# Kernel optimization log

Hardware: AMD Instinct MI355X
Metric: run time of the kernel (lower is better)

Reference implementation:

```python
import jax, jax.numpy as jnp
import numpy as np

B, I, C, L, KS = 16, 64, 128, 16384, 5
CA_K = 5
K_CR = 76      # crucial channels: floor(0.6*128)=76, already even
EPS = 1e-5


def conv1d(x, w, pad):
    # x: [N, Cin, L], w: [Cout, Cin, K]
    return jax.lax.conv_general_dilated(
        x, w, window_strides=(1,), padding=[(pad, pad)],
        dimension_numbers=('NCH', 'OIH', 'NCH'))


def bn(x, g, b, m, v):
    # eval-mode BatchNorm1d over channel dim of [N, C, L]
    inv = g / jnp.sqrt(v + EPS)
    return x * inv[None, :, None] + (b - m * inv)[None, :, None]


def setup_inputs() -> dict:
    key = jax.random.key(0)
    ks = jax.random.split(key, 10)
    return {
        'x': jax.random.normal(ks[0], (B, I, L), jnp.float32),
        'conv_w': jax.random.normal(ks[1], (C, I, KS), jnp.float32) / np.sqrt(I * KS).astype(np.float32),
        'conv_b': jax.random.normal(ks[2], (C,), jnp.float32) * 0.01,
        'bn_g': jnp.ones((C,), jnp.float32) + jax.random.normal(ks[3], (C,), jnp.float32) * 0.05,
        'bn_b': jax.random.normal(ks[4], (C,), jnp.float32) * 0.05,
        'bn_m': jax.random.normal(ks[5], (C,), jnp.float32) * 0.05,
        'bn_v': jnp.ones((C,), jnp.float32) + jax.random.uniform(ks[6], (C,), jnp.float32) * 0.1,
        'alpha': jnp.float32(0.5),
        'beta': jnp.float32(0.5),
        'ca_w': jax.random.normal(ks[7], (1, 1, CA_K), jnp.float32) / np.sqrt(CA_K).astype(np.float32),
        'ca_b': jnp.zeros((1,), jnp.float32),
        'sa_w': jax.random.normal(ks[8], (1, 2, 7), jnp.float32) / np.sqrt(14.0).astype(np.float32),
        'sabn_g': jnp.ones((1,), jnp.float32) + jax.random.normal(ks[9], (1,), jnp.float32) * 0.05,
        'sabn_b': jnp.zeros((1,), jnp.float32),
        'sabn_m': jnp.zeros((1,), jnp.float32),
        'sabn_v': jnp.ones((1,), jnp.float32),
    }


def reference(x, conv_w, conv_b, bn_g, bn_b, bn_m, bn_v, alpha, beta,
              ca_w, ca_b, sa_w, sabn_g, sabn_b, sabn_m, sabn_v):
    # ---- conv_layer: Conv1d + BN + ReLU ----
    f = conv1d(x, conv_w, KS // 2) + conv_b[None, :, None]      # [B,C,L]
    f = jax.nn.relu(bn(f, bn_g, bn_b, bn_m, bn_v))

    # ---- ChannelAttention ----
    F_avg = jnp.mean(f, axis=2, keepdims=True)                  # [B,C,1]
    F_max = jnp.max(f, axis=2, keepdims=True)                   # [B,C,1]
    F_add = alpha * F_avg + 0.5 * (F_avg + F_max) + beta * F_max
    z = conv1d(F_add.transpose(0, 2, 1), ca_w, CA_K // 2) + ca_b[None, :, None]  # [B,1,C]
    channel_map = jax.nn.sigmoid(z.transpose(0, 2, 1))          # [B,C,1]

    crf = f * channel_map                                       # channel refined features

    # ---- SpatialAttention: topk channel split + scatter masks ----
    cm = channel_map[:, :, 0]                                   # [B,C]
    _, idx = jax.lax.top_k(cm, K_CR)                            # [B,K_CR]
    cru = jnp.zeros_like(cm).at[jnp.arange(B)[:, None], idx].set(1.0)[:, :, None]  # [B,C,1]
    sub = 1.0 - cru

    cf = cru * crf                                              # crucial features [B,C,L]
    sf = sub * crf                                              # subcrucial features

    c_max = jnp.max(cf, axis=1, keepdims=True)                  # [B,1,L]
    c_avg = jnp.mean(cf, axis=1, keepdims=True) * (C / K_CR)
    s_max = jnp.max(sf, axis=1, keepdims=True)
    s_avg = jnp.mean(sf, axis=1, keepdims=True) * (C / (C - K_CR))

    def gate(mx, av):
        y = conv1d(jnp.concatenate([mx, av], axis=1), sa_w, 3)  # [B,1,L]
        return jax.nn.sigmoid(jax.nn.relu(bn(y, sabn_g, sabn_b, sabn_m, sabn_v)))

    A1 = gate(c_max, c_avg)
    A2 = gate(s_max, s_avg)
    return cf * A1 + sf * A2                                    # [B,C,L]
```

## Files before the change

kernel.cpp:

```cpp
#include <hip/hip_runtime.h>
#include <hip/hip_bf16.h>
#include <math.h>

#define BB 16
#define IC 64
#define CH 128
#define LL 16384
#define KS 5
#define CAK 5
#define KCR 76
#define EPSV 1e-5f
#define NLT2 256

typedef short bf16x8 __attribute__((ext_vector_type(8)));
typedef float f32x16 __attribute__((ext_vector_type(16)));

#define OFF_WPACK 0
#define OFF_BIAS2 40960
#define OFF_PSUM  (OFF_BIAS2 + CH)
#define OFF_PMAX  (OFF_PSUM + BB*CH*NLT2)
#define OFF_CM    (OFF_PMAX + BB*CH*NLT2)
#define OFF_MASK  (OFF_CM + BB*CH)
#define OFF_A1    (OFF_MASK + BB*CH)
#define OFF_A2    (OFF_A1 + BB*LL)

__device__ __forceinline__ unsigned short f2bf(float f) {
    union { float f; unsigned u; } v; v.f = f;
    return (unsigned short)((v.u + 0x7FFFu + ((v.u >> 16) & 1u)) >> 16);
}
__device__ __forceinline__ float bf2f(unsigned short h) {
    union { unsigned u; float f; } v; v.u = ((unsigned)h) << 16;
    return v.f;
}

__global__ void prep_kernel(const float* __restrict__ conv_w, const float* __restrict__ conv_b,
                            const float* __restrict__ bn_g, const float* __restrict__ bn_b,
                            const float* __restrict__ bn_m, const float* __restrict__ bn_v,
                            unsigned short* __restrict__ wpack, float* __restrict__ bias2)
{
    int e = blockIdx.x * 256 + threadIdx.x;
    if (e < 2 * 2 * 2 * 20 * 64 * 8) {
        int j    = e & 7;
        int ln   = (e >> 3) & 63;
        int rest = e >> 9;
        int s    = rest % 20;
        int mt   = (rest / 20) & 1;
        int ch2  = (rest / 40) & 1;
        int ver  = rest / 80;
        int c  = ch2 * 64 + mt * 32 + (ln & 31);
        int kk = s >> 2;
        int i  = (s & 3) * 16 + (ln >> 5) * 8 + j;
        float inv = bn_g[c] * rsqrtf(bn_v[c] + EPSV);
        float w = conv_w[(c * IC + i) * KS + kk] * inv;
        unsigned short h = f2bf(w);
        wpack[e] = (ver == 0) ? h : f2bf(w - bf2f(h));
    }
    if (e < CH) {
        float inv = bn_g[e] * rsqrtf(bn_v[e] + EPSV);
        bias2[e] = (conv_b[e] - bn_m[e]) * inv + bn_b[e];
    }
}

__global__ __launch_bounds__(256, 3)
void conv_mfma_kernel(const float* __restrict__ x,
                      const unsigned short* __restrict__ wpack,
                      const float* __restrict__ bias2,
                      float* __restrict__ f,
                      float* __restrict__ psum, float* __restrict__ pmax)
{
    __shared__ unsigned short xs[136 * 128];
    const int b   = blockIdx.x;
    const int lt  = blockIdx.y;
    const int l0  = lt * 128;
    const int tid = threadIdx.x;
    const int ln  = tid & 63;
    const int wv  = __builtin_amdgcn_readfirstlane(tid >> 6);

    const float* xb = x + (size_t)b * (IC * LL);
    const int ibase = wv * 16;
    #pragma unroll
    for (int g = 0; g < 3; ++g) {
        int row = g * 64 + ln;
        int l   = l0 - 4 + row;
        if (row < 136) {
            bool vl = (l >= 0) && (l < LL);
            float v[16];
            #pragma unroll
            for (int q = 0; q < 16; ++q)
                v[q] = vl ? xb[(size_t)(ibase + q) * LL + l] : 0.0f;
            int rs = row & 7;
            #pragma unroll
            for (int q2 = 0; q2 < 4; ++q2) {
                unsigned short h[4], lo[4];
                #pragma unroll
                for (int j = 0; j < 4; ++j) {
                    float vv = v[q2 * 4 + j];
                    h[j]  = f2bf(vv);
                    lo[j] = f2bf(vv - bf2f(h[j]));
                }
                int i0   = ibase + q2 * 4;
                int cc   = (i0 >> 3) ^ rs;
                int epos = row * 128 + cc * 8 + (i0 & 7);
                uint2 wh, wl;
                wh.x = (unsigned)h[0]  | ((unsigned)h[1]  << 16);
                wh.y = (unsigned)h[2]  | ((unsigned)h[3]  << 16);
                wl.x = (unsigned)lo[0] | ((unsigned)lo[1] << 16);
                wl.y = (unsigned)lo[2] | ((unsigned)lo[3] << 16);
                *(uint2*)&xs[epos]      = wh;
                *(uint2*)&xs[epos + 64] = wl;
            }
        }
    }
    __syncthreads();

    const int ch2  = wv >> 1;
    const int lh   = wv & 1;
    const int ln31 = ln & 31;
    const int hi   = ln >> 5;
    const int rowbase = lh * 64 + ln31 + 2;

    const unsigned short* wp  = wpack + (size_t)ln * 8;
    const unsigned short* pA0 = wp + (size_t)((ch2 * 2 + 0) * 20) * 512;
    const unsigned short* pA1 = wp + (size_t)((ch2 * 2 + 1) * 20) * 512;
    const unsigned short* pA2 = wp + (size_t)(((2 + ch2) * 2 + 0) * 20) * 512;
    const unsigned short* pA3 = wp + (size_t)(((2 + ch2) * 2 + 1) * 20) * 512;

    f32x16 acc[2][2];
    #pragma unroll
    for (int mt = 0; mt < 2; ++mt)
        #pragma unroll
        for (int nt = 0; nt < 2; ++nt)
            #pragma unroll
            for (int r = 0; r < 16; ++r) acc[mt][nt][r] = 0.0f;

    auto loadA = [&](bf16x8* Av, int s) {
        Av[0] = *(const bf16x8*)(pA0 + (size_t)s * 512);
        Av[1] = *(const bf16x8*)(pA1 + (size_t)s * 512);
        Av[2] = *(const bf16x8*)(pA2 + (size_t)s * 512);
        Av[3] = *(const bf16x8*)(pA3 + (size_t)s * 512);
    };
    auto loadB = [&](bf16x8* Bv, int s) {
        int kk = s >> 2, iq = s & 3;
        int r0 = rowbase + kk;
        int r1 = r0 + 32;
        int c0 = ((iq << 1) + hi) ^ (r0 & 7);
        int c1 = ((iq << 1) + hi) ^ (r1 & 7);
        Bv[0] = *(const bf16x8*)&xs[r0 * 128 + c0 * 8];
        Bv[1] = *(const bf16x8*)&xs[r0 * 128 + 64 + c0 * 8];
        Bv[2] = *(const bf16x8*)&xs[r1 * 128 + c1 * 8];
        Bv[3] = *(const bf16x8*)&xs[r1 * 128 + 64 + c1 * 8];
    };
    auto compute = [&](const bf16x8* Av, const bf16x8* Bv) {
        acc[0][0] = __builtin_amdgcn_mfma_f32_32x32x16_bf16(Av[0], Bv[0], acc[0][0], 0, 0, 0);
        acc[1][0] = __builtin_amdgcn_mfma_f32_32x32x16_bf16(Av[1], Bv[0], acc[1][0], 0, 0, 0);
        acc[0][0] = __builtin_amdgcn_mfma_f32_32x32x16_bf16(Av[0], Bv[1], acc[0][0], 0, 0, 0);
        acc[1][0] = __builtin_amdgcn_mfma_f32_32x32x16_bf16(Av[1], Bv[1], acc[1][0], 0, 0, 0);
        acc[0][0] = __builtin_amdgcn_mfma_f32_32x32x16_bf16(Av[2], Bv[0], acc[0][0], 0, 0, 0);
        acc[1][0] = __builtin_amdgcn_mfma_f32_32x32x16_bf16(Av[3], Bv[0], acc[1][0], 0, 0, 0);
        acc[0][1] = __builtin_amdgcn_mfma_f32_32x32x16_bf16(Av[0], Bv[2], acc[0][1], 0, 0, 0);
        acc[1][1] = __builtin_amdgcn_mfma_f32_32x32x16_bf16(Av[1], Bv[2], acc[1][1], 0, 0, 0);
        acc[0][1] = __builtin_amdgcn_mfma_f32_32x32x16_bf16(Av[0], Bv[3], acc[0][1], 0, 0, 0);
        acc[1][1] = __builtin_amdgcn_mfma_f32_32x32x16_bf16(Av[1], Bv[3], acc[1][1], 0, 0, 0);
        acc[0][1] = __builtin_amdgcn_mfma_f32_32x32x16_bf16(Av[2], Bv[2], acc[0][1], 0, 0, 0);
        acc[1][1] = __builtin_amdgcn_mfma_f32_32x32x16_bf16(Av[3], Bv[2], acc[1][1], 0, 0, 0);
    };

    bf16x8 Aa[4], Ab[4], Ba[4], Bb[4];
    loadA(Aa, 0); loadB(Ba, 0);
    for (int s2 = 0; s2 < 10; ++s2) {
        int s = 2 * s2;
        loadA(Ab, s + 1); loadB(Bb, s + 1);
        compute(Aa, Ba);
        int sn = (s + 2 < 20) ? (s + 2) : 19;
        loadA(Aa, sn); loadB(Ba, sn);
        compute(Ab, Bb);
    }

    const int lgbase = l0 + lh * 64 + ln31;
    #pragma unroll
    for (int mt = 0; mt < 2; ++mt) {
        #pragma unroll
        for (int nt = 0; nt < 2; ++nt) {
            #pragma unroll
            for (int r = 0; r < 16; ++r) {
                int c = ch2 * 64 + mt * 32 + (r & 3) + 8 * (r >> 2) + 4 * hi;
                float fv = fmaxf(acc[mt][nt][r] + bias2[c], 0.0f);
                f[((size_t)(b * CH + c)) * LL + lgbase + nt * 32] = fv;
                acc[mt][nt][r] = fv;
            }
        }
    }
    #pragma unroll
    for (int mt = 0; mt < 2; ++mt) {
        #pragma unroll
        for (int r = 0; r < 16; ++r) {
            float s = acc[mt][0][r] + acc[mt][1][r];
            float m = fmaxf(acc[mt][0][r], acc[mt][1][r]);
            #pragma unroll
            for (int off = 1; off <= 16; off <<= 1) {
                s += __shfl_xor(s, off, 64);
                m = fmaxf(m, __shfl_xor(m, off, 64));
            }
            if (ln31 == 0) {
                int c   = ch2 * 64 + mt * 32 + (r & 3) + 8 * (r >> 2) + 4 * hi;
                int lt2 = lt * 2 + lh;
                psum[(b * CH + c) * NLT2 + lt2] = s;
                pmax[(b * CH + c) * NLT2 + lt2] = m;
            }
        }
    }
}

__global__ void chan_kernel(const float* __restrict__ psum, const float* __restrict__ pmax,
                            const float* __restrict__ alpha, const float* __restrict__ beta,
                            const float* __restrict__ ca_w, const float* __restrict__ ca_b,
                            float* __restrict__ cm, float* __restrict__ maskv)
{
    int b = blockIdx.x;
    int c = threadIdx.x;
    const float* ps = psum + (b * CH + c) * NLT2;
    const float* pm = pmax + (b * CH + c) * NLT2;
    float s = 0.0f, m = 0.0f;
    for (int t = 0; t < NLT2; ++t) { s += ps[t]; m = fmaxf(m, pm[t]); }
    float favg = s * (1.0f / LL);
    float fadd = (alpha[0] + 0.5f) * favg + (beta[0] + 0.5f) * m;

    __shared__ float fa[CH];
    __shared__ float cms[CH];
    fa[c] = fadd;
    __syncthreads();

    float z = ca_b[0];
    #pragma unroll
    for (int k = 0; k < CAK; ++k) {
        int cc = c + k - 2;
        float v = (cc >= 0 && cc < CH) ? fa[cc] : 0.0f;
        z = fmaf(ca_w[k], v, z);
    }
    float cmv = 1.0f / (1.0f + expf(-z));
    cms[c] = cmv;
    __syncthreads();

    int rank = 0;
    for (int cc = 0; cc < CH; ++cc) {
        float o = cms[cc];
        rank += (o > cmv || (o == cmv && cc < c)) ? 1 : 0;
    }
    cm[b * CH + c] = cmv;
    maskv[b * CH + c] = (rank < KCR) ? 1.0f : 0.0f;
}

__global__ __launch_bounds__(256)
void stats_gate_kernel(const float* __restrict__ f, const float* __restrict__ cm,
                       const float* __restrict__ maskv, const float* __restrict__ sa_w,
                       const float* __restrict__ sabn_g, const float* __restrict__ sabn_b,
                       const float* __restrict__ sabn_m, const float* __restrict__ sabn_v,
                       float* __restrict__ A1, float* __restrict__ A2)
{
    __shared__ float cms[CH], mks[CH];
    __shared__ float st[4][264];
    int b   = blockIdx.x;
    int l0  = blockIdx.y * 256;
    int tid = threadIdx.x;
    if (tid < CH) { cms[tid] = cm[b * CH + tid]; mks[tid] = maskv[b * CH + tid]; }
    __syncthreads();

    for (int idx = tid; idx < 262; idx += 256) {
        int l = l0 - 3 + idx;
        float cmx = 0.f, csm = 0.f, smx = 0.f, ssm = 0.f;
        if (l >= 0 && l < LL) {
            const float* fb = f + (size_t)b * CH * LL + l;
            #pragma unroll 4
            for (int c = 0; c < CH; ++c) {
                float v  = fb[(size_t)c * LL] * cms[c];
                float mk = mks[c];
                float vs = v * mk;
                float vu = v - vs;
                cmx = fmaxf(cmx, vs);
                smx = fmaxf(smx, vu);
                csm += vs;
                ssm += vu;
            }
        }
        st[0][idx] = cmx;
        st[1][idx] = csm * (1.0f / KCR);
        st[2][idx] = smx;
        st[3][idx] = ssm * (1.0f / (CH - KCR));
    }
    __syncthreads();

    float inv = sabn_g[0] * rsqrtf(sabn_v[0] + EPSV);
    float bb2 = sabn_b[0] - sabn_m[0] * inv;
    float y1 = 0.f, y2 = 0.f;
    #pragma unroll
    for (int k = 0; k < 7; ++k) {
        float wm = sa_w[k], wa = sa_w[7 + k];
        y1 = fmaf(wm, st[0][tid + k], fmaf(wa, st[1][tid + k], y1));
        y2 = fmaf(wm, st[2][tid + k], fmaf(wa, st[3][tid + k], y2));
    }
    float t1 = fmaxf(y1 * inv + bb2, 0.f);
    float t2 = fmaxf(y2 * inv + bb2, 0.f);
    A1[b * LL + l0 + tid] = 1.0f / (1.0f + expf(-t1));
    A2[b * LL + l0 + tid] = 1.0f / (1.0f + expf(-t2));
}

__global__ __launch_bounds__(256)
void final_kernel(float* __restrict__ out, const float* __restrict__ cm,
                  const float* __restrict__ maskv,
                  const float* __restrict__ A1, const float* __restrict__ A2)
{
    int g = blockIdx.x * 256 + threadIdx.x;
    size_t idx4 = (size_t)g * 4;
    int l  = (int)(idx4 & (LL - 1));
    int bc = (int)(idx4 >> 14);
    int b  = bc >> 7;
    float cmv = cm[bc];
    float mk  = maskv[bc];
    const float* Ap = (mk > 0.5f) ? A1 : A2;
    float4 a = *(const float4*)&Ap[b * LL + l];
    float4 v = *(const float4*)&out[idx4];
    v.x *= cmv * a.x;
    v.y *= cmv * a.y;
    v.z *= cmv * a.z;
    v.w *= cmv * a.w;
    *(float4*)&out[idx4] = v;
}

extern "C" void kernel_launch(void* const* d_in, const int* in_sizes, int n_in,
                              void* d_out, int out_size, void* d_ws, size_t ws_size,
                              hipStream_t stream)
{
    const float* x      = (const float*)d_in[0];
    const float* conv_w = (const float*)d_in[1];
    const float* conv_b = (const float*)d_in[2];
    const float* bn_g   = (const float*)d_in[3];
    const float* bn_b   = (const float*)d_in[4];
    const float* bn_m   = (const float*)d_in[5];
    const float* bn_v   = (const float*)d_in[6];
    const float* alpha  = (const float*)d_in[7];
    const float* beta   = (const float*)d_in[8];
    const float* ca_w   = (const float*)d_in[9];
    const float* ca_b   = (const float*)d_in[10];
    const float* sa_w   = (const float*)d_in[11];
    const float* sabn_g = (const float*)d_in[12];
    const float* sabn_b = (const float*)d_in[13];
    const float* sabn_m = (const float*)d_in[14];
    const float* sabn_v = (const float*)d_in[15];

    float* out = (float*)d_out;
    float* ws  = (float*)d_ws;

    unsigned short* wpack = (unsigned short*)(ws + OFF_WPACK);
    float* bias2 = ws + OFF_BIAS2;
    float* psum  = ws + OFF_PSUM;
    float* pmax  = ws + OFF_PMAX;
    float* cmv_  = ws + OFF_CM;
    float* mskv  = ws + OFF_MASK;
    float* A1p   = ws + OFF_A1;
    float* A2p   = ws + OFF_A2;

    prep_kernel<<<320, 256, 0, stream>>>(conv_w, conv_b, bn_g, bn_b, bn_m, bn_v, wpack, bias2);

    conv_mfma_kernel<<<dim3(BB, 128), 256, 0, stream>>>(x, wpack, bias2, out, psum, pmax);

    chan_kernel<<<BB, CH, 0, stream>>>(psum, pmax, alpha, beta, ca_w, ca_b, cmv_, mskv);

    stats_gate_kernel<<<dim3(BB, 64), 256, 0, stream>>>(out, cmv_, mskv, sa_w,
                                                        sabn_g, sabn_b, sabn_m, sabn_v, A1p, A2p);

    final_kernel<<<(BB * CH * LL / 4 + 255) / 256, 256, 0, stream>>>(out, cmv_, mskv, A1p, A2p);
}
```

Before: 190.7 us.

## Fuse spatial gate with final scaling and persist conv blocks over four tiles

The conv kernel now handles four consecutive 128-wide L tiles per block. It double-buffers the shared x staging so the next tile's global loads overlap the epilogue, keeps the channel sums and maxes in registers, and writes 3-element halo values to a side buffer. The stats/gate kernel and the final scaling kernel are merged into one kernel. It caches each 256-column slab of f in shared memory as fp16, reads halo columns from the side buffer, and writes the output in place. This removes a full extra read and write pass over f plus the A1/A2 buffers. In exchange it adds fp16 rounding of the intermediate features and raises the shared memory each block needs.

```diff
diff --git a/kernel.cpp b/kernel.cpp
--- a/kernel.cpp
+++ b/kernel.cpp
@@ -10,7 +10,7 @@
 #define CAK 5
 #define KCR 76
 #define EPSV 1e-5f
-#define NLT2 256
+#define NLT2 64
 
 typedef short bf16x8 __attribute__((ext_vector_type(8)));
 typedef float f32x16 __attribute__((ext_vector_type(16)));
@@ -21,8 +21,7 @@
 #define OFF_PMAX  (OFF_PSUM + BB*CH*NLT2)
 #define OFF_CM    (OFF_PMAX + BB*CH*NLT2)
 #define OFF_MASK  (OFF_CM + BB*CH)
-#define OFF_A1    (OFF_MASK + BB*CH)
-#define OFF_A2    (OFF_A1 + BB*LL)
+#define OFF_HB    (OFF_MASK + BB*CH)
 
 __device__ __forceinline__ unsigned short f2bf(float f) {
     union { float f; unsigned u; } v; v.f = f;
@@ -31,6 +30,14 @@
 __device__ __forceinline__ float bf2f(unsigned short h) {
     union { unsigned u; float f; } v; v.u = ((unsigned)h) << 16;
     return v.f;
+}
+__device__ __forceinline__ unsigned short f2h(float f) {
+    _Float16 h = (_Float16)f;
+    return __builtin_bit_cast(unsigned short, h);
+}
+__device__ __forceinline__ float h2f(unsigned short u) {
+    _Float16 h = __builtin_bit_cast(_Float16, u);
+    return (float)h;
 }
 
 __global__ void prep_kernel(const float* __restrict__ conv_w, const float* __restrict__ conv_b,
@@ -61,33 +68,35 @@
     }
 }
 
-__global__ __launch_bounds__(256, 3)
+__global__ __launch_bounds__(256, 2)
 void conv_mfma_kernel(const float* __restrict__ x,
                       const unsigned short* __restrict__ wpack,
                       const float* __restrict__ bias2,
                       float* __restrict__ f,
-                      float* __restrict__ psum, float* __restrict__ pmax)
+                      float* __restrict__ psum, float* __restrict__ pmax,
+                      float* __restrict__ hb)
 {
-    __shared__ unsigned short xs[136 * 128];
-    const int b   = blockIdx.x;
-    const int lt  = blockIdx.y;
-    const int l0  = lt * 128;
+    __shared__ unsigned short xs[2 * 136 * 128];
+    const int ltg = blockIdx.x;
+    const int b   = blockIdx.y;
     const int tid = threadIdx.x;
     const int ln  = tid & 63;
     const int wv  = __builtin_amdgcn_readfirstlane(tid >> 6);
+    const int ibase = wv * 16;
 
     const float* xb = x + (size_t)b * (IC * LL);
-    const int ibase = wv * 16;
-    #pragma unroll
-    for (int g = 0; g < 3; ++g) {
+
+    auto sld = [&](float* v, int l0t, int g) {
         int row = g * 64 + ln;
-        int l   = l0 - 4 + row;
+        int l   = l0t - 4 + row;
+        bool vl = (row < 136) && (l >= 0) && (l < LL);
+        #pragma unroll
+        for (int q = 0; q < 16; ++q)
+            v[q] = vl ? xb[(size_t)(ibase + q) * LL + l] : 0.0f;
+    };
+    auto swr = [&](const float* v, unsigned short* buf, int g) {
+        int row = g * 64 + ln;
         if (row < 136) {
-            bool vl = (l >= 0) && (l < LL);
-            float v[16];
-            #pragma unroll
-            for (int q = 0; q < 16; ++q)
-                v[q] = vl ? xb[(size_t)(ibase + q) * LL + l] : 0.0f;
             int rs = row & 7;
             #pragma unroll
             for (int q2 = 0; q2 < 4; ++q2) {
@@ -106,12 +115,11 @@
                 wh.y = (unsigned)h[2]  | ((unsigned)h[3]  << 16);
                 wl.x = (unsigned)lo[0] | ((unsigned)lo[1] << 16);
                 wl.y = (unsigned)lo[2] | ((unsigned)lo[3] << 16);
-                *(uint2*)&xs[epos]      = wh;
-                *(uint2*)&xs[epos + 64] = wl;
+                *(uint2*)&buf[epos]      = wh;
+                *(uint2*)&buf[epos + 64] = wl;
             }
         }
-    }
-    __syncthreads();
+    };
 
     const int ch2  = wv >> 1;
     const int lh   = wv & 1;
@@ -125,31 +133,36 @@
     const unsigned short* pA2 = wp + (size_t)(((2 + ch2) * 2 + 0) * 20) * 512;
     const unsigned short* pA3 = wp + (size_t)(((2 + ch2) * 2 + 1) * 20) * 512;
 
-    f32x16 acc[2][2];
-    #pragma unroll
-    for (int mt = 0; mt < 2; ++mt)
-        #pragma unroll
-        for (int nt = 0; nt < 2; ++nt)
-            #pragma unroll
-            for (int r = 0; r < 16; ++r) acc[mt][nt][r] = 0.0f;
-
     auto loadA = [&](bf16x8* Av, int s) {
         Av[0] = *(const bf16x8*)(pA0 + (size_t)s * 512);
         Av[1] = *(const bf16x8*)(pA1 + (size_t)s * 512);
         Av[2] = *(const bf16x8*)(pA2 + (size_t)s * 512);
         Av[3] = *(const bf16x8*)(pA3 + (size_t)s * 512);
     };
-    auto loadB = [&](bf16x8* Bv, int s) {
+    auto loadB = [&](bf16x8* Bv, const unsigned short* buf, int s) {
         int kk = s >> 2, iq = s & 3;
         int r0 = rowbase + kk;
         int r1 = r0 + 32;
         int c0 = ((iq << 1) + hi) ^ (r0 & 7);
         int c1 = ((iq << 1) + hi) ^ (r1 & 7);
-        Bv[0] = *(const bf16x8*)&xs[r0 * 128 + c0 * 8];
-        Bv[1] = *(const bf16x8*)&xs[r0 * 128 + 64 + c0 * 8];
-        Bv[2] = *(const bf16x8*)&xs[r1 * 128 + c1 * 8];
-        Bv[3] = *(const bf16x8*)&xs[r1 * 128 + 64 + c1 * 8];
-    };
+        Bv[0] = *(const bf16x8*)&buf[r0 * 128 + c0 * 8];
+        Bv[1] = *(const bf16x8*)&buf[r0 * 128 + 64 + c0 * 8];
+        Bv[2] = *(const bf16x8*)&buf[r1 * 128 + c1 * 8];
+        Bv[3] = *(const bf16x8*)&buf[r1 * 128 + 64 + c1 * 8];
+    };
+
+    f32x16 acc[2][2];
+    float sacc[2][16], macc[2][16];
+    #pragma unroll
+    for (int mt = 0; mt < 2; ++mt) {
+        #pragma unroll
+        for (int r = 0; r < 16; ++r) { sacc[mt][r] = 0.f; macc[mt][r] = 0.f; }
+        #pragma unroll
+        for (int nt = 0; nt < 2; ++nt)
+            #pragma unroll
+            for (int r = 0; r < 16; ++r) acc[mt][nt][r] = 0.0f;
+    }
+
     auto compute = [&](const bf16x8* Av, const bf16x8* Bv) {
         acc[0][0] = __builtin_amdgcn_mfma_f32_32x32x16_bf16(Av[0], Bv[0], acc[0][0], 0, 0, 0);
         acc[1][0] = __builtin_amdgcn_mfma_f32_32x32x16_bf16(Av[1], Bv[0], acc[1][0], 0, 0, 0);
@@ -165,47 +178,74 @@
         acc[1][1] = __builtin_amdgcn_mfma_f32_32x32x16_bf16(Av[3], Bv[2], acc[1][1], 0, 0, 0);
     };
 
-    bf16x8 Aa[4], Ab[4], Ba[4], Bb[4];
-    loadA(Aa, 0); loadB(Ba, 0);
-    for (int s2 = 0; s2 < 10; ++s2) {
-        int s = 2 * s2;
-        loadA(Ab, s + 1); loadB(Bb, s + 1);
-        compute(Aa, Ba);
-        int sn = (s + 2 < 20) ? (s + 2) : 19;
-        loadA(Aa, sn); loadB(Ba, sn);
-        compute(Ab, Bb);
-    }
-
-    const int lgbase = l0 + lh * 64 + ln31;
-    #pragma unroll
-    for (int mt = 0; mt < 2; ++mt) {
+    auto epi = [&](int mt, int l0t) {
         #pragma unroll
         for (int nt = 0; nt < 2; ++nt) {
+            int lg = l0t + lh * 64 + ln31 + nt * 32;
+            int lm = lg & 255;
+            bool hs = (lm < 3) || (lm >= 253);
+            int hslot = (lg >> 8) * 6 + (lm < 3 ? lm : lm - 250);
             #pragma unroll
             for (int r = 0; r < 16; ++r) {
                 int c = ch2 * 64 + mt * 32 + (r & 3) + 8 * (r >> 2) + 4 * hi;
                 float fv = fmaxf(acc[mt][nt][r] + bias2[c], 0.0f);
-                f[((size_t)(b * CH + c)) * LL + lgbase + nt * 32] = fv;
-                acc[mt][nt][r] = fv;
+                f[((size_t)(b * CH + c)) * LL + lg] = fv;
+                if (hs) hb[((size_t)(b * CH + c)) * 384 + hslot] = fv;
+                sacc[mt][r] += fv;
+                macc[mt][r] = fmaxf(macc[mt][r], fv);
+                acc[mt][nt][r] = 0.0f;
             }
         }
-    }
+    };
+
+    {
+        float sv[16];
+        sld(sv, ltg * 512, 0); swr(sv, xs, 0);
+        sld(sv, ltg * 512, 1); swr(sv, xs, 1);
+        sld(sv, ltg * 512, 2); swr(sv, xs, 2);
+    }
+    __syncthreads();
+
+    for (int t = 0; t < 4; ++t) {
+        unsigned short* cb = xs + (t & 1) * (136 * 128);
+        unsigned short* nb = xs + ((t + 1) & 1) * (136 * 128);
+        const int l0t = ltg * 512 + t * 128;
+        const bool more = (t < 3);
+
+        bf16x8 Af[2][4], Bf[2][4];
+        loadA(Af[0], 0); loadB(Bf[0], cb, 0);
+        #pragma unroll
+        for (int s = 0; s < 20; ++s) {
+            if (s < 19) { loadA(Af[(s + 1) & 1], s + 1); loadB(Bf[(s + 1) & 1], cb, s + 1); }
+            compute(Af[s & 1], Bf[s & 1]);
+        }
+
+        float sv[16];
+        if (more) sld(sv, l0t + 128, 0);
+        epi(0, l0t);
+        if (more) { swr(sv, nb, 0); sld(sv, l0t + 128, 1); }
+        epi(1, l0t);
+        if (more) { swr(sv, nb, 1); sld(sv, l0t + 128, 2); }
+        if (more) swr(sv, nb, 2);
+        __syncthreads();
+    }
+
     #pragma unroll
     for (int mt = 0; mt < 2; ++mt) {
         #pragma unroll
         for (int r = 0; r < 16; ++r) {
-            float s = acc[mt][0][r] + acc[mt][1][r];
-            float m = fmaxf(acc[mt][0][r], acc[mt][1][r]);
+            float s = sacc[mt][r];
+            float m = macc[mt][r];
             #pragma unroll
             for (int off = 1; off <= 16; off <<= 1) {
                 s += __shfl_xor(s, off, 64);
                 m = fmaxf(m, __shfl_xor(m, off, 64));
             }
             if (ln31 == 0) {
-                int c   = ch2 * 64 + mt * 32 + (r & 3) + 8 * (r >> 2) + 4 * hi;
-                int lt2 = lt * 2 + lh;
-                psum[(b * CH + c) * NLT2 + lt2] = s;
-                pmax[(b * CH + c) * NLT2 + lt2] = m;
+                int c    = ch2 * 64 + mt * 32 + (r & 3) + 8 * (r >> 2) + 4 * hi;
+                int slot = ltg * 2 + lh;
+                psum[(b * CH + c) * NLT2 + slot] = s;
+                pmax[(b * CH + c) * NLT2 + slot] = m;
             }
         }
     }
@@ -250,18 +290,20 @@
     maskv[b * CH + c] = (rank < KCR) ? 1.0f : 0.0f;
 }
 
-__global__ __launch_bounds__(256)
-void stats_gate_kernel(const float* __restrict__ f, const float* __restrict__ cm,
-                       const float* __restrict__ maskv, const float* __restrict__ sa_w,
-                       const float* __restrict__ sabn_g, const float* __restrict__ sabn_b,
-                       const float* __restrict__ sabn_m, const float* __restrict__ sabn_v,
-                       float* __restrict__ A1, float* __restrict__ A2)
+__global__ __launch_bounds__(256, 2)
+void sgf_kernel(float* fo, const float* __restrict__ hb,
+                const float* __restrict__ cm, const float* __restrict__ maskv,
+                const float* __restrict__ sa_w,
+                const float* __restrict__ sabn_g, const float* __restrict__ sabn_b,
+                const float* __restrict__ sabn_m, const float* __restrict__ sabn_v)
 {
+    __shared__ unsigned short f16[CH][256];
+    __shared__ float st[4][262];
     __shared__ float cms[CH], mks[CH];
-    __shared__ float st[4][264];
-    int b   = blockIdx.x;
-    int l0  = blockIdx.y * 256;
-    int tid = threadIdx.x;
+    const int g   = blockIdx.x;
+    const int b   = blockIdx.y;
+    const int l0  = g * 256;
+    const int tid = threadIdx.x;
     if (tid < CH) { cms[tid] = cm[b * CH + tid]; mks[tid] = maskv[b * CH + tid]; }
     __syncthreads();
 
@@ -269,10 +311,20 @@
         int l = l0 - 3 + idx;
         float cmx = 0.f, csm = 0.f, smx = 0.f, ssm = 0.f;
         if (l >= 0 && l < LL) {
-            const float* fb = f + (size_t)b * CH * LL + l;
+            bool inter = (idx >= 3) && (idx < 259);
+            const float* fb  = fo + (size_t)b * CH * LL + l;
+            int lm = l & 255;
+            const float* hbb = hb + ((size_t)b * CH) * 384 + (l >> 8) * 6 + (lm < 3 ? lm : lm - 250);
             #pragma unroll 4
             for (int c = 0; c < CH; ++c) {
-                float v  = fb[(size_t)c * LL] * cms[c];
+                float v;
+                if (inter) {
+                    v = fb[(size_t)c * LL];
+                    f16[c][idx - 3] = f2h(v);
+                } else {
+                    v = hbb[(size_t)c * 384];
+                }
+                v *= cms[c];
                 float mk = mks[c];
                 float vs = v * mk;
                 float vu = v - vs;
@@ -300,30 +352,16 @@
     }
     float t1 = fmaxf(y1 * inv + bb2, 0.f);
     float t2 = fmaxf(y2 * inv + bb2, 0.f);
-    A1[b * LL + l0 + tid] = 1.0f / (1.0f + expf(-t1));
-    A2[b * LL + l0 + tid] = 1.0f / (1.0f + expf(-t2));
-}
-
-__global__ __launch_bounds__(256)
-void final_kernel(float* __restrict__ out, const float* __restrict__ cm,
-                  const float* __restrict__ maskv,
-                  const float* __restrict__ A1, const float* __restrict__ A2)
-{
-    int g = blockIdx.x * 256 + threadIdx.x;
-    size_t idx4 = (size_t)g * 4;
-    int l  = (int)(idx4 & (LL - 1));
-    int bc = (int)(idx4 >> 14);
-    int b  = bc >> 7;
-    float cmv = cm[bc];
-    float mk  = maskv[bc];
-    const float* Ap = (mk > 0.5f) ? A1 : A2;
-    float4 a = *(const float4*)&Ap[b * LL + l];
-    float4 v = *(const float4*)&out[idx4];
-    v.x *= cmv * a.x;
-    v.y *= cmv * a.y;
-    v.z *= cmv * a.z;
-    v.w *= cmv * a.w;
-    *(float4*)&out[idx4] = v;
+    float A1 = 1.0f / (1.0f + expf(-t1));
+    float A2 = 1.0f / (1.0f + expf(-t2));
+
+    float* ob = fo + (size_t)b * CH * LL + l0 + tid;
+    #pragma unroll 4
+    for (int c = 0; c < CH; ++c) {
+        float v = h2f(f16[c][tid]) * cms[c];
+        float a = (mks[c] > 0.5f) ? A1 : A2;
+        ob[(size_t)c * LL] = v * a;
+    }
 }
 
 extern "C" void kernel_launch(void* const* d_in, const int* in_sizes, int n_in,
@@ -356,17 +394,14 @@
     float* pmax  = ws + OFF_PMAX;
     float* cmv_  = ws + OFF_CM;
     float* mskv  = ws + OFF_MASK;
-    float* A1p   = ws + OFF_A1;
-    float* A2p   = ws + OFF_A2;
+    float* hbp   = ws + OFF_HB;
 
     prep_kernel<<<320, 256, 0, stream>>>(conv_w, conv_b, bn_g, bn_b, bn_m, bn_v, wpack, bias2);
 
-    conv_mfma_kernel<<<dim3(BB, 128), 256, 0, stream>>>(x, wpack, bias2, out, psum, pmax);
+    conv_mfma_kernel<<<dim3(32, BB), 256, 0, stream>>>(x, wpack, bias2, out, psum, pmax, hbp);
 
     chan_kernel<<<BB, CH, 0, stream>>>(psum, pmax, alpha, beta, ca_w, ca_b, cmv_, mskv);
 
-    stats_gate_kernel<<<dim3(BB, 64), 256, 0, stream>>>(out, cmv_, mskv, sa_w,
-                                                        sabn_g, sabn_b, sabn_m, sabn_v, A1p, A2p);
-
-    final_kernel<<<(BB * CH * LL / 4 + 255) / 256, 256, 0, stream>>>(out, cmv_, mskv, A1p, A2p);
-}
+    sgf_kernel<<<dim3(64, BB), 256, 0, stream>>>(out, hbp, cmv_, mskv, sa_w,
+                                                 sabn_g, sabn_b, sabn_m, sabn_v);
+}
```

Measured after the change: 722.6 us. 279% more time.
